# Kernel tuning notes

Measured on AMD Instinct MI355X. Metric: run time of the kernel, lower is better.

The kernel has to match this reference:

```python
import jax, jax.numpy as jnp
import numpy as np

N_NODES = 100000
N_EDGES = 1600000
IN_FEAT = 128
EMBED = 64
N_LAYERS = 3
N_CENTROID = 100
N_CLASS = 10
EPS = 1e-12


def setup_inputs() -> dict:
    key = jax.random.key(0)
    ks = jax.random.split(key, 8)
    x = jax.random.normal(ks[0], (N_NODES, IN_FEAT), dtype=jnp.float32)
    edge_index = jax.random.randint(ks[1], (2, N_EDGES), 0, N_NODES, dtype=jnp.int64)
    W_embed = jax.random.normal(ks[2], (EMBED, IN_FEAT), dtype=jnp.float32) / np.sqrt(IN_FEAT)
    W_gcn = jax.random.normal(ks[3], (N_LAYERS, EMBED, EMBED), dtype=jnp.float32) / np.sqrt(EMBED)
    b_gcn = jnp.zeros((N_LAYERS, EMBED), dtype=jnp.float32)
    centroids = jax.random.normal(ks[4], (N_CENTROID, EMBED), dtype=jnp.float32)
    W_out = jax.random.normal(ks[5], (N_CLASS, N_CENTROID), dtype=jnp.float32) / np.sqrt(N_CENTROID)
    b_out = jnp.zeros((N_CLASS,), dtype=jnp.float32)
    return {"x": x, "edge_index": edge_index, "W_embed": W_embed, "W_gcn": W_gcn,
            "b_gcn": b_gcn, "centroids": centroids, "W_out": W_out, "b_out": b_out}


def _gcn_norm(edge_index, n, dtype):
    # add self loops, compute symmetric D^{-1/2}(A+I)D^{-1/2} edge weights
    loops = jnp.arange(n, dtype=edge_index.dtype)
    src = jnp.concatenate([edge_index[0], loops])
    dst = jnp.concatenate([edge_index[1], loops])
    deg = jax.ops.segment_sum(jnp.ones_like(dst, dtype=dtype), dst, num_segments=n)
    dinv = jax.lax.rsqrt(jnp.maximum(deg, 1.0))
    norm = dinv[src] * dinv[dst]  # [E+N]
    return src, dst, norm


def reference(x, edge_index, W_embed, W_gcn, b_gcn, centroids, W_out, b_out):
    n = x.shape[0]
    src, dst, norm = _gcn_norm(edge_index, n, x.dtype)
    # Euclidean manifold: log/exp are identity
    h = x @ W_embed.T  # [N, D]
    for l in range(W_gcn.shape[0]):
        hw = h @ W_gcn[l].T                                   # [N, D]
        msg = hw[src] * norm[:, None]                         # gather  [E+N, D]
        h = jax.ops.segment_sum(msg, dst, num_segments=n)     # scatter [N, D]
        h = jax.nn.relu(h + b_gcn[l])
    # centroid distances: ||h_i - c_k|| via expanded quadratic (avoids [N,K,D])
    h2 = jnp.sum(h * h, axis=-1, keepdims=True)               # [N, 1]
    c2 = jnp.sum(centroids * centroids, axis=-1)[None, :]     # [1, K]
    d2 = jnp.maximum(h2 + c2 - 2.0 * (h @ centroids.T), 0.0)  # [N, K]
    dist = jnp.sqrt(d2 + EPS)
    pooled = dist.mean(axis=0)                                # [K] graph pooling
    return pooled @ W_out.T + b_out                           # [num_class]
```

## Files before the change

kernel.cpp:

```cpp
#include <hip/hip_runtime.h>
#include <hip/hip_bf16.h>

typedef unsigned int uint32;
typedef float floatx2 __attribute__((ext_vector_type(2)));
typedef __attribute__((ext_vector_type(8))) short bf16x8;
typedef __attribute__((ext_vector_type(4))) float f32x4;

#define CHUNK 4096


__global__ __launch_bounds__(256) void k_bhist(const int* __restrict__ dst,
                                               int* __restrict__ bcnt,
                                               int E, int NBUCK, int NCH) {
    __shared__ int h[512];
    int c = blockIdx.x, tid = threadIdx.x;
    for (int i = tid; i < NBUCK; i += 256) h[i] = 0;
    __syncthreads();
    int base = c * CHUNK;
#pragma unroll
    for (int k = 0; k < CHUNK / 256; ++k) {
        int e = base + k * 256 + tid;
        if (e < E) atomicAdd(&h[dst[e] >> 8], 1);
    }
    __syncthreads();
    for (int i = tid; i < NBUCK; i += 256) bcnt[(size_t)i * NCH + c] = h[i];
}

__global__ __launch_bounds__(512) void k_bscan1(const int* __restrict__ bcnt,
                                                int* __restrict__ bofs,
                                                int* __restrict__ btot, int NCH) {
    __shared__ int tmp[512];
    int b = blockIdx.x, t = threadIdx.x;
    int v = (t < NCH) ? bcnt[(size_t)b * NCH + t] : 0;
    tmp[t] = v;
    __syncthreads();
    for (int off = 1; off < 512; off <<= 1) {
        int u = (t >= off) ? tmp[t - off] : 0;
        __syncthreads();
        tmp[t] += u;
        __syncthreads();
    }
    if (t < NCH) bofs[(size_t)b * NCH + t] = tmp[t] - v;
    if (t == 511) btot[b] = tmp[511];
}

__global__ __launch_bounds__(512) void k_bscan2(const int* __restrict__ btot,
                                                int* __restrict__ bbase, int nb,
                                                uint32* __restrict__ sent0,
                                                uint32* __restrict__ sent1) {
    __shared__ int tmp[512];
    int t = threadIdx.x;
    if (t < 8) { sent0[t] = 0; sent1[t] = 0; }
    int v = (t < nb) ? btot[t] : 0;
    tmp[t] = v;
    __syncthreads();
    for (int off = 1; off < 512; off <<= 1) {
        int u = (t >= off) ? tmp[t - off] : 0;
        __syncthreads();
        tmp[t] += u;
        __syncthreads();
    }
    if (t < nb) bbase[t] = tmp[t] - v;
    if (t == nb - 1) bbase[nb] = tmp[t];
}

__global__ __launch_bounds__(256) void k_bscatter(const int* __restrict__ ei,
                                                  const int* __restrict__ bbase,
                                                  const int* __restrict__ bofs,
                                                  uint32* __restrict__ ebuf,
                                                  int E, int NBUCK, int NCH) {
    __shared__ int cur[512];
    int c = blockIdx.x, tid = threadIdx.x;
    for (int i = tid; i < NBUCK; i += 256)
        cur[i] = bbase[i] + bofs[(size_t)i * NCH + c];
    __syncthreads();
    int base = c * CHUNK;
#pragma unroll
    for (int k = 0; k < CHUNK / 256; ++k) {
        int e = base + k * 256 + tid;
        if (e < E) {
            int s = ei[e];
            int d = ei[E + e];
            int p = atomicAdd(&cur[d >> 8], 1);
            ebuf[p] = (uint32)s | ((uint32)(d & 255) << 20);
        }
    }
}

__global__ __launch_bounds__(256) void k_bsort(const uint32* __restrict__ ebuf,
                                               const int* __restrict__ bbase,
                                               int* __restrict__ ssrc,
                                               int2* __restrict__ rc,
                                               float* __restrict__ dinv, int N) {
    __shared__ int h[256];
    __shared__ int sc[256];
    __shared__ int cur[256];
    int b = blockIdx.x, tid = threadIdx.x;
    int beg = bbase[b], end = bbase[b + 1];
    h[tid] = 0;
    __syncthreads();
    for (int j = beg + tid; j < end; j += 256)
        atomicAdd(&h[(ebuf[j] >> 20) & 255], 1);
    __syncthreads();
    int v = h[tid];
    sc[tid] = v;
    __syncthreads();
    for (int off = 1; off < 256; off <<= 1) {
        int u = (tid >= off) ? sc[tid - off] : 0;
        __syncthreads();
        sc[tid] += u;
        __syncthreads();
    }
    int rowbase = beg + sc[tid] - v;
    cur[tid] = rowbase;
    int d = b * 256 + tid;
    if (d < N) {
        rc[d] = make_int2(rowbase, v);
        dinv[d] = rsqrtf((float)(v + 1));
    }
    __syncthreads();
    for (int j = beg + tid; j < end; j += 256) {
        uint32 w = ebuf[j];
        int p = atomicAdd(&cur[(w >> 20) & 255], 1);
        ssrc[p] = (int)(w & 0xFFFFFu);
    }
}


__device__ __forceinline__ short f2bf(float f) {
    __hip_bfloat16 b = __float2bfloat16(f);
    return __builtin_bit_cast(short, b);
}

__device__ __forceinline__ float bf2f(short s) {
    uint32 u = ((uint32)(unsigned short)s) << 16;
    return __builtin_bit_cast(float, u);
}

__device__ __forceinline__ bf16x8 pack_bf16x8(float4 v0, float4 v1) {
    bf16x8 r;
    r[0] = f2bf(v0.x); r[1] = f2bf(v0.y); r[2] = f2bf(v0.z); r[3] = f2bf(v0.w);
    r[4] = f2bf(v1.x); r[5] = f2bf(v1.y); r[6] = f2bf(v1.z); r[7] = f2bf(v1.w);
    return r;
}


__global__ __launch_bounds__(256) void k_embed(const float* __restrict__ x,
                                               const float* __restrict__ We,
                                               short* __restrict__ h, int N) {
    int lane = threadIdx.x & 63;
    int w = threadIdx.x >> 6;
    int l15 = lane & 15;
    int lg = lane >> 4;

    bf16x8 B[4][4];
#pragma unroll
    for (int ct = 0; ct < 4; ++ct) {
        const float* wr = We + (size_t)(ct * 16 + l15) * 128 + lg * 8;
#pragma unroll
        for (int ks = 0; ks < 4; ++ks) {
            float4 v0 = *(const float4*)(wr + ks * 32);
            float4 v1 = *(const float4*)(wr + ks * 32 + 4);
            B[ct][ks] = pack_bf16x8(v0, v1);
        }
    }

    int rowbase = blockIdx.x * 256 + w * 64;

    f32x4 acc[4][4];
#pragma unroll
    for (int rt = 0; rt < 4; ++rt)
#pragma unroll
        for (int ct = 0; ct < 4; ++ct)
            acc[rt][ct] = (f32x4){0.f, 0.f, 0.f, 0.f};

#pragma unroll
    for (int ks = 0; ks < 4; ++ks) {
#pragma unroll
        for (int rt = 0; rt < 4; ++rt) {
            int row = rowbase + rt * 16 + l15;
            row = (row < N) ? row : (N - 1);
            const float* xr = x + (size_t)row * 128 + ks * 32 + lg * 8;
            float4 v0 = *(const float4*)xr;
            float4 v1 = *(const float4*)(xr + 4);
            bf16x8 a = pack_bf16x8(v0, v1);
#pragma unroll
            for (int ct = 0; ct < 4; ++ct)
                acc[rt][ct] = __builtin_amdgcn_mfma_f32_16x16x32_bf16(
                    a, B[ct][ks], acc[rt][ct], 0, 0, 0);
        }
    }

#pragma unroll
    for (int rt = 0; rt < 4; ++rt) {
        int row0 = rowbase + rt * 16 + lg * 4;
#pragma unroll
        for (int r = 0; r < 4; ++r) {
            int row = row0 + r;
            if (row < N) {
#pragma unroll
                for (int ct = 0; ct < 4; ++ct)
                    h[(size_t)row * 64 + ct * 16 + l15] = f2bf(acc[rt][ct][r]);
            }
        }
    }
}


__global__ __launch_bounds__(256) void k_gcn(const short* __restrict__ hin,
                                             const float* __restrict__ Wg,
                                             const float* __restrict__ dinv,
                                             uint32* __restrict__ tab0,
                                             uint32* __restrict__ tab1, int N) {
    int lane = threadIdx.x & 63;
    int w = threadIdx.x >> 6;
    int l15 = lane & 15, lg = lane >> 4;

    bf16x8 A[4][2];
#pragma unroll
    for (int rt = 0; rt < 4; ++rt) {
        const float* wr = Wg + (size_t)(rt * 16 + l15) * 64 + lg * 8;
#pragma unroll
        for (int ks = 0; ks < 2; ++ks) {
            float4 v0 = *(const float4*)(wr + ks * 32);
            float4 v1 = *(const float4*)(wr + ks * 32 + 4);
            A[rt][ks] = pack_bf16x8(v0, v1);
        }
    }

    int nodebase = blockIdx.x * 256 + w * 64;

#pragma unroll
    for (int nt = 0; nt < 4; ++nt) {
        int node = nodebase + nt * 16 + l15;
        int nodec = (node < N) ? node : (N - 1);
        const short* hr = hin + ((size_t)nodec << 6) + lg * 8;

        bf16x8 Bf0 = *(const bf16x8*)(hr);
        bf16x8 Bf1 = *(const bf16x8*)(hr + 32);

        f32x4 acc[4];
#pragma unroll
        for (int rt = 0; rt < 4; ++rt) acc[rt] = (f32x4){0.f, 0.f, 0.f, 0.f};
#pragma unroll
        for (int rt = 0; rt < 4; ++rt)
            acc[rt] = __builtin_amdgcn_mfma_f32_16x16x32_bf16(A[rt][0], Bf0, acc[rt], 0, 0, 0);
#pragma unroll
        for (int rt = 0; rt < 4; ++rt)
            acc[rt] = __builtin_amdgcn_mfma_f32_16x16x32_bf16(A[rt][1], Bf1, acc[rt], 0, 0, 0);

        float s = dinv[nodec];
        if (node < N) {
#pragma unroll
            for (int rt = 0; rt < 4; ++rt) {
                int u = 0;
                u = __builtin_amdgcn_cvt_pk_fp8_f32(acc[rt][0] * s, acc[rt][1] * s, u, false);
                u = __builtin_amdgcn_cvt_pk_fp8_f32(acc[rt][2] * s, acc[rt][3] * s, u, true);
                uint32* tp = (rt < 2) ? tab0 : tab1;
                tp[(size_t)node * 8 + (rt & 1) * 4 + lg] = u;
            }
        }
    }
}


__global__ __launch_bounds__(256) void k_agg(const int2* __restrict__ rc,
                                             const int* __restrict__ ssrc,
                                             const float* __restrict__ dinv,
                                             const uint2* __restrict__ tab0,
                                             const uint2* __restrict__ tab1,
                                             short* __restrict__ hA,
                                             const float* __restrict__ biasl,
                                             int N, int E) {
    int half = blockIdx.x & 1;
    int bb = blockIdx.x >> 1;
    const uint2* tabh = half ? tab1 : tab0;
    int lane = threadIdx.x & 63;
    int wid = threadIdx.x >> 6;
    int q = lane & 3;
    int g = lane >> 2;
    int dbase = (bb * 4 + wid) * 16;
    if (dbase >= N) return;

    int2 r = rc[min(dbase + (lane & 15), N - 1)];
    int beg = __shfl(r.x, g);
    int deg = __shfl(r.y, g);
    int dg = dbase + g;
    if (dg >= N) deg = 0;

    floatx2 a01 = {0.f, 0.f}, a23 = {0.f, 0.f}, a45 = {0.f, 0.f}, a67 = {0.f, 0.f};
    auto accum = [&](uint2 v) {
        a01 += __builtin_amdgcn_cvt_pk_f32_fp8((int)v.x, false);
        a23 += __builtin_amdgcn_cvt_pk_f32_fp8((int)v.x, true);
        a45 += __builtin_amdgcn_cvt_pk_f32_fp8((int)v.y, false);
        a67 += __builtin_amdgcn_cvt_pk_f32_fp8((int)v.y, true);
    };

    accum(tabh[(size_t)((dg < N) ? dg : N) * 4 + q]);

    int m = deg;
    m = max(m, __shfl_xor(m, 4));
    m = max(m, __shfl_xor(m, 8));
    m = max(m, __shfl_xor(m, 16));
    m = max(m, __shfl_xor(m, 32));
    int maxd = __builtin_amdgcn_readfirstlane(m);

    int base4 = lane & 60;
    for (int j = 0; j < maxd; j += 16) {
        int i0 = beg + j + q;
        int i1 = i0 + 4;
        int i2 = i0 + 8;
        int i3 = i0 + 12;
        int ev0 = ssrc[i0 < E ? i0 : 0];
        int ev1 = ssrc[i1 < E ? i1 : 0];
        int ev2 = ssrc[i2 < E ? i2 : 0];
        int ev3 = ssrc[i3 < E ? i3 : 0];
        int t0  = __shfl(ev0, base4 | 0);
        int t1  = __shfl(ev0, base4 | 1);
        int t2  = __shfl(ev0, base4 | 2);
        int t3  = __shfl(ev0, base4 | 3);
        int t4  = __shfl(ev1, base4 | 0);
        int t5  = __shfl(ev1, base4 | 1);
        int t6  = __shfl(ev1, base4 | 2);
        int t7  = __shfl(ev1, base4 | 3);
        int t8  = __shfl(ev2, base4 | 0);
        int t9  = __shfl(ev2, base4 | 1);
        int ta  = __shfl(ev2, base4 | 2);
        int tb  = __shfl(ev2, base4 | 3);
        int tc  = __shfl(ev3, base4 | 0);
        int td  = __shfl(ev3, base4 | 1);
        int te  = __shfl(ev3, base4 | 2);
        int tf  = __shfl(ev3, base4 | 3);
        t0 = (j +  0 < deg) ? t0 : N;
        t1 = (j +  1 < deg) ? t1 : N;
        t2 = (j +  2 < deg) ? t2 : N;
        t3 = (j +  3 < deg) ? t3 : N;
        t4 = (j +  4 < deg) ? t4 : N;
        t5 = (j +  5 < deg) ? t5 : N;
        t6 = (j +  6 < deg) ? t6 : N;
        t7 = (j +  7 < deg) ? t7 : N;
        t8 = (j +  8 < deg) ? t8 : N;
        t9 = (j +  9 < deg) ? t9 : N;
        ta = (j + 10 < deg) ? ta : N;
        tb = (j + 11 < deg) ? tb : N;
        tc = (j + 12 < deg) ? tc : N;
        td = (j + 13 < deg) ? td : N;
        te = (j + 14 < deg) ? te : N;
        tf = (j + 15 < deg) ? tf : N;
        uint2 v0 = tabh[(size_t)t0 * 4 + q];
        uint2 v1 = tabh[(size_t)t1 * 4 + q];
        uint2 v2 = tabh[(size_t)t2 * 4 + q];
        uint2 v3 = tabh[(size_t)t3 * 4 + q];
        uint2 v4 = tabh[(size_t)t4 * 4 + q];
        uint2 v5 = tabh[(size_t)t5 * 4 + q];
        uint2 v6 = tabh[(size_t)t6 * 4 + q];
        uint2 v7 = tabh[(size_t)t7 * 4 + q];
        uint2 v8 = tabh[(size_t)t8 * 4 + q];
        uint2 v9 = tabh[(size_t)t9 * 4 + q];
        uint2 va = tabh[(size_t)ta * 4 + q];
        uint2 vb = tabh[(size_t)tb * 4 + q];
        uint2 vc = tabh[(size_t)tc * 4 + q];
        uint2 vd = tabh[(size_t)td * 4 + q];
        uint2 ve = tabh[(size_t)te * 4 + q];
        uint2 vf = tabh[(size_t)tf * 4 + q];
        accum(v0); accum(v1); accum(v2); accum(v3);
        accum(v4); accum(v5); accum(v6); accum(v7);
        accum(v8); accum(v9); accum(va); accum(vb);
        accum(vc); accum(vd); accum(ve); accum(vf);
    }

    if (dg < N) {
        float dd = dinv[dg];
        const float* bias = biasl + half * 32;
        float4 b0 = *(const float4*)(bias + q * 8);
        float4 b1 = *(const float4*)(bias + q * 8 + 4);
        bf16x8 o;
        o[0] = f2bf(fmaxf(fmaf(dd, a01.x, b0.x), 0.f));
        o[1] = f2bf(fmaxf(fmaf(dd, a01.y, b0.y), 0.f));
        o[2] = f2bf(fmaxf(fmaf(dd, a23.x, b0.z), 0.f));
        o[3] = f2bf(fmaxf(fmaf(dd, a23.y, b0.w), 0.f));
        o[4] = f2bf(fmaxf(fmaf(dd, a45.x, b1.x), 0.f));
        o[5] = f2bf(fmaxf(fmaf(dd, a45.y, b1.y), 0.f));
        o[6] = f2bf(fmaxf(fmaf(dd, a67.x, b1.z), 0.f));
        o[7] = f2bf(fmaxf(fmaf(dd, a67.y, b1.w), 0.f));
        __builtin_nontemporal_store(o, (bf16x8*)(hA + (size_t)dg * 64 + half * 32 + q * 8));
    }
}


__global__ __launch_bounds__(256) void k_cent(const short* __restrict__ hin,
                                              const float* __restrict__ C,
                                              float* __restrict__ partials, int N) {
    __shared__ float pool4[4][112];
    __shared__ float h2_s[128];
    int tid = threadIdx.x;
    int lane = tid & 63, w = tid >> 6;
    int l15 = lane & 15, lg = lane >> 4;

    bf16x8 B[7][2];
    float c2r[7];
#pragma unroll
    for (int ct = 0; ct < 7; ++ct) {
        int col = ct * 16 + l15;
        float c2p = 0.f;
#pragma unroll
        for (int ks = 0; ks < 2; ++ks) {
            float4 v0 = make_float4(0.f, 0.f, 0.f, 0.f);
            float4 v1 = make_float4(0.f, 0.f, 0.f, 0.f);
            if (col < 100) {
                const float* cr = C + (size_t)col * 64 + ks * 32 + lg * 8;
                v0 = *(const float4*)cr;
                v1 = *(const float4*)(cr + 4);
            }
            B[ct][ks] = pack_bf16x8(v0, v1);
            c2p = fmaf(v0.x, v0.x, c2p); c2p = fmaf(v0.y, v0.y, c2p);
            c2p = fmaf(v0.z, v0.z, c2p); c2p = fmaf(v0.w, v0.w, c2p);
            c2p = fmaf(v1.x, v1.x, c2p); c2p = fmaf(v1.y, v1.y, c2p);
            c2p = fmaf(v1.z, v1.z, c2p); c2p = fmaf(v1.w, v1.w, c2p);
        }
        c2p += __shfl_xor(c2p, 16);
        c2p += __shfl_xor(c2p, 32);
        c2r[ct] = c2p;
    }

    int rowbase = blockIdx.x * 128 + w * 32;

    f32x4 acc[2][7];
#pragma unroll
    for (int rt = 0; rt < 2; ++rt)
#pragma unroll
        for (int ct = 0; ct < 7; ++ct)
            acc[rt][ct] = (f32x4){0.f, 0.f, 0.f, 0.f};

#pragma unroll
    for (int rt = 0; rt < 2; ++rt) {
        int row = rowbase + rt * 16 + l15;
        int rowc = (row < N) ? row : (N - 1);
        const short* hr = hin + ((size_t)rowc << 6) + lg * 8;
        bf16x8 a0 = *(const bf16x8*)(hr);
        bf16x8 a1 = *(const bf16x8*)(hr + 32);

        float h2p = 0.f;
#pragma unroll
        for (int j = 0; j < 8; ++j) {
            float v0 = bf2f(a0[j]);
            float v1 = bf2f(a1[j]);
            h2p = fmaf(v0, v0, h2p);
            h2p = fmaf(v1, v1, h2p);
        }
        h2p += __shfl_xor(h2p, 16);
        h2p += __shfl_xor(h2p, 32);
        if (lg == 0) h2_s[w * 32 + rt * 16 + l15] = h2p;

#pragma unroll
        for (int ct = 0; ct < 7; ++ct)
            acc[rt][ct] = __builtin_amdgcn_mfma_f32_16x16x32_bf16(
                a0, B[ct][0], acc[rt][ct], 0, 0, 0);
#pragma unroll
        for (int ct = 0; ct < 7; ++ct)
            acc[rt][ct] = __builtin_amdgcn_mfma_f32_16x16x32_bf16(
                a1, B[ct][1], acc[rt][ct], 0, 0, 0);
    }

    float S[7] = {0.f, 0.f, 0.f, 0.f, 0.f, 0.f, 0.f};
#pragma unroll
    for (int rt = 0; rt < 2; ++rt) {
#pragma unroll
        for (int r = 0; r < 4; ++r) {
            int row = rowbase + rt * 16 + lg * 4 + r;
            float h2v = h2_s[w * 32 + rt * 16 + lg * 4 + r];
            bool rv = row < N;
#pragma unroll
            for (int ct = 0; ct < 7; ++ct) {
                int col = ct * 16 + l15;
                float G = acc[rt][ct][r];
                float d2 = fmaxf(h2v + c2r[ct] - 2.f * G, 0.f);
                float xx = d2 + 1e-12f;
                float dist = xx * __frsqrt_rn(xx);
                S[ct] += (rv && col < 100) ? dist : 0.f;
            }
        }
    }
#pragma unroll
    for (int ct = 0; ct < 7; ++ct) {
        float s = S[ct];
        s += __shfl_xor(s, 16);
        s += __shfl_xor(s, 32);
        if (lg == 0) pool4[w][ct * 16 + l15] = s;
    }
    __syncthreads();
    if (tid < 112) {
        float s = pool4[0][tid] + pool4[1][tid] + pool4[2][tid] + pool4[3][tid];
        partials[(size_t)blockIdx.x * 128 + tid] = s;
    }
}


__global__ __launch_bounds__(1024) void k_out(const float* __restrict__ partials, int nb,
                                              const float* __restrict__ Wout,
                                              const float* __restrict__ bout,
                                              float* __restrict__ out, float invN) {
    __shared__ float ps[8][112];
    int t = threadIdx.x & 127, g = threadIdx.x >> 7;
    if (t < 112) {
        float s0 = 0.f, s1 = 0.f, s2 = 0.f, s3 = 0.f;
        float s4 = 0.f, s5 = 0.f, s6 = 0.f, s7 = 0.f;
        int b = g;
        for (; b + 56 < nb; b += 64) {
            s0 += partials[(size_t)(b     ) * 128 + t];
            s1 += partials[(size_t)(b +  8) * 128 + t];
            s2 += partials[(size_t)(b + 16) * 128 + t];
            s3 += partials[(size_t)(b + 24) * 128 + t];
            s4 += partials[(size_t)(b + 32) * 128 + t];
            s5 += partials[(size_t)(b + 40) * 128 + t];
            s6 += partials[(size_t)(b + 48) * 128 + t];
            s7 += partials[(size_t)(b + 56) * 128 + t];
        }
        for (; b < nb; b += 8) s0 += partials[(size_t)b * 128 + t];
        ps[g][t] = ((s0 + s1) + (s2 + s3)) + ((s4 + s5) + (s6 + s7));
    }
    __syncthreads();
    if (threadIdx.x < 10) {
        int tt = threadIdx.x;
        float s = 0.f;
        for (int k = 0; k < 100; ++k) {
            float p = ps[0][k] + ps[1][k] + ps[2][k] + ps[3][k]
                    + ps[4][k] + ps[5][k] + ps[6][k] + ps[7][k];
            s = fmaf(p, Wout[tt * 100 + k], s);
        }
        out[tt] = s * invN + bout[tt];
    }
}


extern "C" void kernel_launch(void* const* d_in, const int* in_sizes, int n_in,
                              void* d_out, int out_size, void* d_ws, size_t ws_size,
                              hipStream_t stream) {
    const float* x    = (const float*)d_in[0];
    const int*   ei   = (const int*)d_in[1];
    const float* We   = (const float*)d_in[2];
    const float* Wg   = (const float*)d_in[3];
    const float* bg   = (const float*)d_in[4];
    const float* C    = (const float*)d_in[5];
    const float* Wout = (const float*)d_in[6];
    const float* bout = (const float*)d_in[7];
    float*       out  = (float*)d_out;

    const int N = in_sizes[0] / 128;
    const int E = in_sizes[1] / 2;
    const int NBUCK = (N + 255) >> 8;
    const int NCH = (E + CHUNK - 1) / CHUNK;
    const int NBC = (N + 127) / 128;
    const int NBA = (N + 63) / 64;

    char* ws = (char*)d_ws;
    size_t off = 0;
    auto alloc = [&](size_t bytes) { void* p = ws + off; off += (bytes + 511) & ~(size_t)511; return p; };
    float*  dinv   = (float*)alloc((size_t)N * 4);
    int2*   rc     = (int2*) alloc((size_t)N * 8);
    int*    bcnt   = (int*)  alloc((size_t)NBUCK * NCH * 4);
    int*    bofs   = (int*)  alloc((size_t)NBUCK * NCH * 4);
    int*    btot   = (int*)  alloc((size_t)NBUCK * 4);
    int*    bbase  = (int*)  alloc((size_t)(NBUCK + 1) * 4);
    uint32* ebuf   = (uint32*)alloc((size_t)E * 4);
    int*    ssrc   = (int*)  alloc((size_t)(E + 64) * 4);
    short*  hA     = (short*)alloc((size_t)N * 64 * 2);
    uint32* tab0   = (uint32*)alloc((size_t)(N + 1) * 32);
    uint32* tab1   = (uint32*)alloc((size_t)(N + 1) * 32);
    float*  partials = (float*)alloc((size_t)NBC * 128 * 4);

    k_bhist<<<NCH, 256, 0, stream>>>(ei + E, bcnt, E, NBUCK, NCH);
    k_bscan1<<<NBUCK, 512, 0, stream>>>(bcnt, bofs, btot, NCH);
    k_bscan2<<<1, 512, 0, stream>>>(btot, bbase, NBUCK,
                                    tab0 + (size_t)N * 8, tab1 + (size_t)N * 8);
    k_bscatter<<<NCH, 256, 0, stream>>>(ei, bbase, bofs, ebuf, E, NBUCK, NCH);
    k_bsort<<<NBUCK, 256, 0, stream>>>(ebuf, bbase, ssrc, rc, dinv, N);

    k_embed<<<(N + 255) / 256, 256, 0, stream>>>(x, We, hA, N);

    for (int l = 0; l < 3; ++l) {
        k_gcn<<<(N + 255) / 256, 256, 0, stream>>>(hA, Wg + (size_t)l * 64 * 64,
                                                   dinv, tab0, tab1, N);
        k_agg<<<2 * NBA, 256, 0, stream>>>(rc, ssrc, dinv, (const uint2*)tab0,
                                           (const uint2*)tab1, hA,
                                           bg + (size_t)l * 64, N, E);
    }

    k_cent<<<NBC, 256, 0, stream>>>(hA, C, partials, N);

    k_out<<<1, 1024, 0, stream>>>(partials, NBC, Wout, bout, out, 1.0f / (float)N);
}
```

Baseline: 309.2 us.

## Sort destination nodes by degree within buckets to balance aggregation wavefronts

The bucket sort kernel now also counting-sorts the 256 nodes of each bucket by in-degree and writes a permutation array. The aggregation kernel reads that permutation so each wavefront handles 16 nodes of similar degree, cutting the idle lanes caused by looping to the group's maximum degree. In exchange it adds a permutation load, an indirect row lookup and less contiguous destination writes.

```diff
diff --git a/kernel.cpp b/kernel.cpp
--- a/kernel.cpp
+++ b/kernel.cpp
@@ -87,11 +87,13 @@
     }
 }
 
+
 __global__ __launch_bounds__(256) void k_bsort(const uint32* __restrict__ ebuf,
                                                const int* __restrict__ bbase,
                                                int* __restrict__ ssrc,
                                                int2* __restrict__ rc,
-                                               float* __restrict__ dinv, int N) {
+                                               float* __restrict__ dinv,
+                                               int* __restrict__ perm, int N) {
     __shared__ int h[256];
     __shared__ int sc[256];
     __shared__ int cur[256];
@@ -124,6 +126,26 @@
         int p = atomicAdd(&cur[(w >> 20) & 255], 1);
         ssrc[p] = (int)(w & 0xFFFFFu);
     }
+
+    __syncthreads();
+    h[tid] = 0;
+    __syncthreads();
+    int bin = (v < 255) ? v : 255;
+    atomicAdd(&h[bin], 1);
+    __syncthreads();
+    int vv = h[tid];
+    sc[tid] = vv;
+    __syncthreads();
+    for (int off = 1; off < 256; off <<= 1) {
+        int u = (tid >= off) ? sc[tid - off] : 0;
+        __syncthreads();
+        sc[tid] += u;
+        __syncthreads();
+    }
+    cur[tid] = sc[tid] - vv;
+    __syncthreads();
+    int p = atomicAdd(&cur[bin], 1);
+    perm[b * 256 + p] = d;
 }
 
 
@@ -269,6 +291,7 @@
                                              const float* __restrict__ dinv,
                                              const uint2* __restrict__ tab0,
                                              const uint2* __restrict__ tab1,
+                                             const int* __restrict__ perm,
                                              short* __restrict__ hA,
                                              const float* __restrict__ biasl,
                                              int N, int E) {
@@ -282,10 +305,12 @@
     int dbase = (bb * 4 + wid) * 16;
     if (dbase >= N) return;
 
-    int2 r = rc[min(dbase + (lane & 15), N - 1)];
+    int pd = perm[dbase + (lane & 15)];
+    int pdc = (pd < N) ? pd : (N - 1);
+    int2 r = rc[pdc];
     int beg = __shfl(r.x, g);
     int deg = __shfl(r.y, g);
-    int dg = dbase + g;
+    int dg = __shfl(pd, g);
     if (dg >= N) deg = 0;
 
     floatx2 a01 = {0.f, 0.f}, a23 = {0.f, 0.f}, a45 = {0.f, 0.f}, a67 = {0.f, 0.f};
@@ -558,6 +583,7 @@
     auto alloc = [&](size_t bytes) { void* p = ws + off; off += (bytes + 511) & ~(size_t)511; return p; };
     float*  dinv   = (float*)alloc((size_t)N * 4);
     int2*   rc     = (int2*) alloc((size_t)N * 8);
+    int*    perm   = (int*)  alloc((size_t)NBUCK * 256 * 4);
     int*    bcnt   = (int*)  alloc((size_t)NBUCK * NCH * 4);
     int*    bofs   = (int*)  alloc((size_t)NBUCK * NCH * 4);
     int*    btot   = (int*)  alloc((size_t)NBUCK * 4);
@@ -574,7 +600,7 @@
     k_bscan2<<<1, 512, 0, stream>>>(btot, bbase, NBUCK,
                                     tab0 + (size_t)N * 8, tab1 + (size_t)N * 8);
     k_bscatter<<<NCH, 256, 0, stream>>>(ei, bbase, bofs, ebuf, E, NBUCK, NCH);
-    k_bsort<<<NBUCK, 256, 0, stream>>>(ebuf, bbase, ssrc, rc, dinv, N);
+    k_bsort<<<NBUCK, 256, 0, stream>>>(ebuf, bbase, ssrc, rc, dinv, perm, N);
 
     k_embed<<<(N + 255) / 256, 256, 0, stream>>>(x, We, hA, N);
 
@@ -582,7 +608,7 @@
         k_gcn<<<(N + 255) / 256, 256, 0, stream>>>(hA, Wg + (size_t)l * 64 * 64,
                                                    dinv, tab0, tab1, N);
         k_agg<<<2 * NBA, 256, 0, stream>>>(rc, ssrc, dinv, (const uint2*)tab0,
-                                           (const uint2*)tab1, hA,
+                                           (const uint2*)tab1, perm, hA,
                                            bg + (size_t)l * 64, N, E);
     }
 
```

Result: slower. 332.1 us (+7.4%).
